# Optimization experiments

Measured on AMD Instinct MI355X. Metric: run time of the kernel, lower is better.

Reference implementation:

```python
import jax, jax.numpy as jnp
import numpy as np

N = 100000
E = 1600000
D_IN = 128
D_HID = 128
D_OUT = 128
HEADS = 4
NEG_SLOPE = 0.2  # PyG GATConv default leaky_relu slope


def setup_inputs() -> dict:
    key = jax.random.key(0)
    ks = jax.random.split(key, 16)
    ch1 = D_HID // HEADS
    ch2 = D_OUT // HEADS
    inp = {
        "x": jax.random.normal(ks[0], (N, D_IN), dtype=jnp.float32),
        "edge_index": jax.random.randint(ks[1], (2, E), 0, N, dtype=jnp.int64),
        # conv1 params
        "W1": jax.random.normal(ks[2], (D_IN, HEADS * ch1), dtype=jnp.float32) * 0.05,
        "a1_src": jax.random.normal(ks[3], (HEADS, ch1), dtype=jnp.float32) * 0.05,
        "a1_dst": jax.random.normal(ks[4], (HEADS, ch1), dtype=jnp.float32) * 0.05,
        "b1": jnp.zeros((HEADS * ch1,), dtype=jnp.float32),
        # conv2 params
        "W2": jax.random.normal(ks[5], (D_HID, HEADS * ch2), dtype=jnp.float32) * 0.05,
        "a2_src": jax.random.normal(ks[6], (HEADS, ch2), dtype=jnp.float32) * 0.05,
        "a2_dst": jax.random.normal(ks[7], (HEADS, ch2), dtype=jnp.float32) * 0.05,
        "b2": jnp.zeros((HEADS * ch2,), dtype=jnp.float32),
        # residual linear
        "Wr": jax.random.normal(ks[8], (D_IN, D_OUT), dtype=jnp.float32) * 0.05,
        "br": jnp.zeros((D_OUT,), dtype=jnp.float32),
    }
    return inp


def _gat_conv(x, W, a_src, a_dst, bias, src, dst, n_nodes):
    """Single PyG-style GATConv (concat heads, eval-mode / no dropout).
    src/dst already include self loops. x: [N, Din]. Returns [N, H*C]."""
    H, C = a_src.shape
    h = (x @ W).reshape(n_nodes, H, C)                      # [N,H,C]
    s_src = jnp.einsum("nhc,hc->nh", h, a_src)              # [N,H]
    s_dst = jnp.einsum("nhc,hc->nh", h, a_dst)              # [N,H]
    e = s_src[src] + s_dst[dst]                             # [E',H]
    e = jnp.where(e > 0, e, NEG_SLOPE * e)                  # leaky_relu
    # softmax over edges grouped by destination node
    e_max = jax.ops.segment_max(e, dst, num_segments=n_nodes)  # [N,H]
    e_exp = jnp.exp(e - e_max[dst])
    denom = jax.ops.segment_sum(e_exp, dst, num_segments=n_nodes)  # [N,H]
    alpha = e_exp / denom[dst]                              # [E',H]
    msg = alpha[:, :, None] * h[src]                        # [E',H,C]
    out = jax.ops.segment_sum(msg, dst, num_segments=n_nodes)  # [N,H,C]
    return out.reshape(n_nodes, H * C) + bias


def reference(x, edge_index, W1, a1_src, a1_dst, b1, W2, a2_src, a2_dst, b2, Wr, br):
    n_nodes = x.shape[0]
    loops = jnp.arange(n_nodes, dtype=edge_index.dtype)
    src = jnp.concatenate([edge_index[0], loops])           # add_self_loops=True
    dst = jnp.concatenate([edge_index[1], loops])
    h1 = _gat_conv(x, W1, a1_src, a1_dst, b1, src, dst, n_nodes)
    h1 = jax.nn.relu(h1)
    h2 = _gat_conv(h1, W2, a2_src, a2_dst, b2, src, dst, n_nodes)
    return h2 + x @ Wr + br
```

## Files before the change

kernel.cpp:

```cpp
#include <hip/hip_runtime.h>

#define NEG_SLOPE 0.2f

typedef short bf16x8 __attribute__((ext_vector_type(8)));
typedef float f32x4 __attribute__((ext_vector_type(4)));

__device__ __forceinline__ float leaky1(float e) { return e > 0.f ? e : NEG_SLOPE * e; }

__device__ __forceinline__ unsigned short f2bf(float f) {
    unsigned u = __float_as_uint(f);
    u += 0x7fffu + ((u >> 16) & 1u);
    return (unsigned short)(u >> 16);
}

__device__ __forceinline__ void split2(float x, short& h, short& lo) {
    unsigned short hb_ = f2bf(x);
    float hf = __uint_as_float(((unsigned)hb_) << 16);
    h = (short)hb_;
    lo = (short)f2bf(x - hf);
}

#define EPB 4096

__global__ __launch_bounds__(256) void bucket_hist(const int* __restrict__ dst,
                                                   int* __restrict__ gcnt,
                                                   int* __restrict__ relBase,
                                                   int E, int N, int NB) {
    __shared__ int hist[256];
    int t = threadIdx.x, blk = blockIdx.x;
    if (t < NB) hist[t] = 0;
    __syncthreads();
    int e0 = blk * EPB + t;
#pragma unroll 4
    for (int k = 0; k < EPB / 256; ++k) {
        int e = e0 + k * 256;
        if (e < E) {
            int d = dst[e];
            if ((unsigned)d < (unsigned)N) atomicAdd(&hist[d >> 9], 1);
        }
    }
    __syncthreads();
    if (t < NB) relBase[blk * NB + t] = atomicAdd(&gcnt[t], hist[t]);
}

__global__ __launch_bounds__(256) void scan_buckets(const int* __restrict__ gcnt,
                                                    int* __restrict__ gboff, int NB) {
    __shared__ int sm[256];
    int t = threadIdx.x;
    int v = (t < NB) ? gcnt[t] : 0;
    sm[t] = v;
    __syncthreads();
#pragma unroll
    for (int o = 1; o < 256; o <<= 1) {
        int u = (t >= o) ? sm[t - o] : 0;
        __syncthreads();
        sm[t] += u;
        __syncthreads();
    }
    if (t < NB) gboff[t] = sm[t] - v;
    if (t == NB - 1) gboff[NB] = sm[t];
}

__global__ __launch_bounds__(256) void bucket_scatter(const int* __restrict__ src,
                                                      const int* __restrict__ dst,
                                                      const int* __restrict__ gboff,
                                                      const int* __restrict__ relBase,
                                                      int2* __restrict__ eb,
                                                      int E, int N, int NB) {
    __shared__ int cur[256];
    int t = threadIdx.x, blk = blockIdx.x;
    if (t < NB) cur[t] = gboff[t] + relBase[blk * NB + t];
    __syncthreads();
    int e0 = blk * EPB + t;
#pragma unroll 4
    for (int k = 0; k < EPB / 256; ++k) {
        int e = e0 + k * 256;
        if (e < E) {
            int d = dst[e];
            if ((unsigned)d < (unsigned)N) {
                int pos = atomicAdd(&cur[d >> 9], 1);
                eb[pos] = make_int2(src[e], d);
            }
        }
    }
}

__global__ __launch_bounds__(512) void csr_build(const int2* __restrict__ eb,
                                                 const int* __restrict__ gboff,
                                                 int* __restrict__ offs,
                                                 int* __restrict__ csr,
                                                 int N, int NB) {
    __shared__ int lcnt[512];
    __shared__ int sm[512];
    __shared__ int cur[512];
    int t = threadIdx.x, b = blockIdx.x;
    lcnt[t] = 0;
    __syncthreads();
    int s0 = gboff[b], s1 = gboff[b + 1];
    for (int e = s0 + t; e < s1; e += 512) atomicAdd(&lcnt[eb[e].y & 511], 1);
    __syncthreads();
    int v = lcnt[t];
    sm[t] = v;
    __syncthreads();
#pragma unroll
    for (int o = 1; o < 512; o <<= 1) {
        int u = (t >= o) ? sm[t - o] : 0;
        __syncthreads();
        sm[t] += u;
        __syncthreads();
    }
    int base = gboff[b] + sm[t] - v;
    cur[t] = base;
    int n0 = (b << 9) + t;
    if (n0 < N) offs[n0] = base;
    if (b == NB - 1 && t == 0) offs[N] = gboff[NB];
    __syncthreads();
    for (int e = s0 + t; e < s1; e += 512) {
        int2 p = eb[e];
        int pos = atomicAdd(&cur[p.y & 511], 1);
        csr[pos] = p.x;
    }
}


__global__ __launch_bounds__(256, 3) void gemm_mfma(const float* __restrict__ X,
                                                    const float* __restrict__ W,
                                                    float* __restrict__ OUT,
                                                    unsigned short* __restrict__ HB,
                                                    const float* __restrict__ bias,
                                                    int accumulate,
                                                    const float* __restrict__ ASrc,
                                                    const float* __restrict__ ADst,
                                                    float* __restrict__ sS4,
                                                    float* __restrict__ sD4, int N) {
    __shared__ __align__(16) char pool[49152];
    short* At2h = (short*)pool;
    short* At2l = (short*)(pool + 8192);
    short* Bt2h = (short*)(pool + 16384);
    short* Bt2l = (short*)(pool + 32768);
    float* outS = (float*)pool;

    int t = threadIdx.x;
    int row0 = blockIdx.x << 6;
    int l = t & 63, w = t >> 6, g = l >> 4, r = l & 15;
    int r0 = w << 4;

    f32x4 acc[8];
#pragma unroll
    for (int nb = 0; nb < 8; ++nb) acc[nb] = (f32x4){0.f, 0.f, 0.f, 0.f};

    int arow = t >> 2, aj = t & 3;
    int growA = row0 + arow;
    if (growA > N - 1) growA = N - 1;
    int bc = t & 127, bh4 = (t >> 7) << 2;

#pragma unroll 1
    for (int ph = 0; ph < 2; ++ph) {
        __syncthreads();
        {
            const float* xp = X + (size_t)growA * 128 + (ph << 6) + (aj << 4);
            float4 x0 = *(const float4*)(xp + 0);
            float4 x1 = *(const float4*)(xp + 4);
            float4 x2 = *(const float4*)(xp + 8);
            float4 x3 = *(const float4*)(xp + 12);
            float v[16] = {x0.x, x0.y, x0.z, x0.w, x1.x, x1.y, x1.z, x1.w,
                           x2.x, x2.y, x2.z, x2.w, x3.x, x3.y, x3.z, x3.w};
#pragma unroll
            for (int u = 0; u < 2; ++u) {
                bf16x8 hv, lv;
#pragma unroll
                for (int i = 0; i < 8; ++i) {
                    short hh, ll;
                    split2(v[u * 8 + i], hh, ll);
                    hv[i] = hh; lv[i] = ll;
                }
                int kg = 2 * aj + u;
                *(bf16x8*)&At2h[(kg * 64 + arow) * 8] = hv;
                *(bf16x8*)&At2l[(kg * 64 + arow) * 8] = lv;
            }
        }
        {
#pragma unroll
            for (int j = 0; j < 4; ++j) {
                int kg = bh4 + j;
                bf16x8 hv, lv;
#pragma unroll
                for (int i = 0; i < 8; ++i) {
                    float f = W[(size_t)((ph << 6) + (kg << 3) + i) * 128 + bc];
                    short hh, ll;
                    split2(f, hh, ll);
                    hv[i] = hh; lv[i] = ll;
                }
                *(bf16x8*)&Bt2h[(kg * 128 + bc) * 8] = hv;
                *(bf16x8*)&Bt2l[(kg * 128 + bc) * 8] = lv;
            }
        }
        __syncthreads();
#pragma unroll
        for (int m = 0; m < 2; ++m) {
            int kb = m << 2;
            bf16x8 ah = *(const bf16x8*)&At2h[((kb + g) * 64 + r0 + r) * 8];
            bf16x8 al = *(const bf16x8*)&At2l[((kb + g) * 64 + r0 + r) * 8];
#pragma unroll
            for (int nb = 0; nb < 8; ++nb) {
                bf16x8 bhv = *(const bf16x8*)&Bt2h[((kb + g) * 128 + (nb << 4) + r) * 8];
                bf16x8 blv = *(const bf16x8*)&Bt2l[((kb + g) * 128 + (nb << 4) + r) * 8];
                acc[nb] = __builtin_amdgcn_mfma_f32_16x16x32_bf16(ah, bhv, acc[nb], 0, 0, 0);
                acc[nb] = __builtin_amdgcn_mfma_f32_16x16x32_bf16(ah, blv, acc[nb], 0, 0, 0);
                acc[nb] = __builtin_amdgcn_mfma_f32_16x16x32_bf16(al, bhv, acc[nb], 0, 0, 0);
            }
        }
    }
    __syncthreads();
#pragma unroll
    for (int nb = 0; nb < 8; ++nb)
#pragma unroll
        for (int reg = 0; reg < 4; ++reg)
            outS[(r0 + (g << 2) + reg) * 129 + (nb << 4) + r] = acc[nb][reg];
    __syncthreads();
    int erow = t & 63, q = t >> 6;
    int grow = row0 + erow;
    if (grow < N) {
        float o[32];
#pragma unroll
        for (int i = 0; i < 32; ++i) o[i] = outS[erow * 129 + (q << 5) + i];
        if (bias) {
#pragma unroll
            for (int i = 0; i < 32; ++i) o[i] += bias[(q << 5) + i];
        }
        if (accumulate) {
#pragma unroll
            for (int i = 0; i < 8; ++i) {
                float4 old = *(const float4*)(OUT + (size_t)grow * 128 + (q << 5) + 4 * i);
                o[4 * i] += old.x; o[4 * i + 1] += old.y;
                o[4 * i + 2] += old.z; o[4 * i + 3] += old.w;
            }
        }
        if (OUT) {
#pragma unroll
            for (int i = 0; i < 8; ++i) {
                float4 v4 = make_float4(o[4 * i], o[4 * i + 1], o[4 * i + 2], o[4 * i + 3]);
                *(float4*)(OUT + (size_t)grow * 128 + (q << 5) + 4 * i) = v4;
            }
        }
        if (HB) {
#pragma unroll
            for (int u = 0; u < 4; ++u) {
                uint4 hv;
                hv.x = (unsigned)f2bf(o[8 * u + 0]) | ((unsigned)f2bf(o[8 * u + 1]) << 16);
                hv.y = (unsigned)f2bf(o[8 * u + 2]) | ((unsigned)f2bf(o[8 * u + 3]) << 16);
                hv.z = (unsigned)f2bf(o[8 * u + 4]) | ((unsigned)f2bf(o[8 * u + 5]) << 16);
                hv.w = (unsigned)f2bf(o[8 * u + 6]) | ((unsigned)f2bf(o[8 * u + 7]) << 16);
                *(uint4*)(HB + (size_t)grow * 128 + (q << 5) + 8 * u) = hv;
            }
        }
        if (ASrc) {
            float ps = 0.f, pd = 0.f;
#pragma unroll
            for (int i = 0; i < 32; ++i) {
                ps = fmaf(o[i], ASrc[(q << 5) + i], ps);
                pd = fmaf(o[i], ADst[(q << 5) + i], pd);
            }
            sS4[(size_t)grow * 4 + q] = ps;
            sD4[(size_t)grow * 4 + q] = pd;
        }
    }
}


__global__ __launch_bounds__(256) void agg7_kernel(const unsigned short* __restrict__ hb,
                                                   const float* __restrict__ sS4,
                                                   const float* __restrict__ sD4,
                                                   const int* __restrict__ offs,
                                                   const int* __restrict__ csr,
                                                   const float* __restrict__ bias,
                                                   float* __restrict__ out,
                                                   int do_relu, int N) {
    int n = (blockIdx.x << 2) + (threadIdx.x >> 6);
    if (n >= N) return;
    int lane = threadIdx.x & 63;
    int q    = lane >> 4;
    int cl   = lane & 15;
    int hd   = cl >> 2;
    unsigned clo = (unsigned)cl << 4;

    float sdh = sD4[(n << 2) + hd];
    float selfw = __expf(leaky1(sS4[(n << 2) + hd] + sdh));

    float acc[8] = {0.f, 0.f, 0.f, 0.f, 0.f, 0.f, 0.f, 0.f};
    float wsum = 0.f;

    int off = offs[n], end = offs[n + 1];
#pragma unroll 1
    for (int base = off; base < end; base += 16) {
        int e0 = base + q;
        int sj[4];
        float wj[4];
#pragma unroll
        for (int i = 0; i < 4; ++i) sj[i] = csr[e0 + (i << 2)];
#pragma unroll
        for (int i = 0; i < 4; ++i) {
            float s = sS4[((unsigned)sj[i] << 2) + hd] + sdh;
            float w = __expf(leaky1(s));
            wj[i] = (e0 + (i << 2) < end) ? w : 0.f;
        }
#pragma unroll
        for (int i = 0; i < 4; ++i) {
            uint4 v = *(const uint4*)((const char*)hb + (((unsigned)sj[i] << 8) + clo));
            float w = wj[i];
            wsum += w;
            acc[0] = fmaf(w, __uint_as_float(v.x << 16), acc[0]);
            acc[1] = fmaf(w, __uint_as_float(v.x & 0xffff0000u), acc[1]);
            acc[2] = fmaf(w, __uint_as_float(v.y << 16), acc[2]);
            acc[3] = fmaf(w, __uint_as_float(v.y & 0xffff0000u), acc[3]);
            acc[4] = fmaf(w, __uint_as_float(v.z << 16), acc[4]);
            acc[5] = fmaf(w, __uint_as_float(v.z & 0xffff0000u), acc[5]);
            acc[6] = fmaf(w, __uint_as_float(v.w << 16), acc[6]);
            acc[7] = fmaf(w, __uint_as_float(v.w & 0xffff0000u), acc[7]);
        }
    }
#pragma unroll
    for (int k = 0; k < 8; ++k) {
        acc[k] += __shfl_xor(acc[k], 16);
        acc[k] += __shfl_xor(acc[k], 32);
    }
    wsum += __shfl_xor(wsum, 16);
    wsum += __shfl_xor(wsum, 32);

    float iv = 1.0f / (wsum + selfw);

    if (q == 0) {
        uint4 hv = *(const uint4*)((const char*)hb + (((unsigned)n << 8) + clo));
        float hs[8];
        hs[0] = __uint_as_float(hv.x << 16);
        hs[1] = __uint_as_float(hv.x & 0xffff0000u);
        hs[2] = __uint_as_float(hv.y << 16);
        hs[3] = __uint_as_float(hv.y & 0xffff0000u);
        hs[4] = __uint_as_float(hv.z << 16);
        hs[5] = __uint_as_float(hv.z & 0xffff0000u);
        hs[6] = __uint_as_float(hv.w << 16);
        hs[7] = __uint_as_float(hv.w & 0xffff0000u);
        float4 b0 = *(const float4*)&bias[8 * cl];
        float4 b1 = *(const float4*)&bias[8 * cl + 4];
        float4 o0, o1;
        o0.x = fmaf(fmaf(selfw, hs[0], acc[0]), iv, b0.x);
        o0.y = fmaf(fmaf(selfw, hs[1], acc[1]), iv, b0.y);
        o0.z = fmaf(fmaf(selfw, hs[2], acc[2]), iv, b0.z);
        o0.w = fmaf(fmaf(selfw, hs[3], acc[3]), iv, b0.w);
        o1.x = fmaf(fmaf(selfw, hs[4], acc[4]), iv, b1.x);
        o1.y = fmaf(fmaf(selfw, hs[5], acc[5]), iv, b1.y);
        o1.z = fmaf(fmaf(selfw, hs[6], acc[6]), iv, b1.z);
        o1.w = fmaf(fmaf(selfw, hs[7], acc[7]), iv, b1.w);
        if (do_relu) {
            o0.x = fmaxf(o0.x, 0.f); o0.y = fmaxf(o0.y, 0.f);
            o0.z = fmaxf(o0.z, 0.f); o0.w = fmaxf(o0.w, 0.f);
            o1.x = fmaxf(o1.x, 0.f); o1.y = fmaxf(o1.y, 0.f);
            o1.z = fmaxf(o1.z, 0.f); o1.w = fmaxf(o1.w, 0.f);
        }
        *(float4*)(out + (size_t)n * 128 + 8 * cl) = o0;
        *(float4*)(out + (size_t)n * 128 + 8 * cl + 4) = o1;
    }
}


extern "C" void kernel_launch(void* const* d_in, const int* in_sizes, int n_in,
                              void* d_out, int out_size, void* d_ws, size_t ws_size,
                              hipStream_t stream) {
    const float* x   = (const float*)d_in[0];
    const int*   ei  = (const int*)d_in[1];
    const float* W1  = (const float*)d_in[2];
    const float* a1s = (const float*)d_in[3];
    const float* a1d = (const float*)d_in[4];
    const float* b1  = (const float*)d_in[5];
    const float* W2  = (const float*)d_in[6];
    const float* a2s = (const float*)d_in[7];
    const float* a2d = (const float*)d_in[8];
    const float* b2  = (const float*)d_in[9];
    const float* Wr  = (const float*)d_in[10];
    const float* br  = (const float*)d_in[11];
    float* out = (float*)d_out;

    int N = in_sizes[0] / 128;
    int E = in_sizes[1] / 2;
    const int* src = ei;
    const int* dst = ei + E;
    int NB = (N + 511) >> 9;
    int ebl = (E + EPB - 1) / EPB;

    char* w = (char*)d_ws;
    size_t p = 0;
    auto take = [&](size_t bytes) -> char* {
        char* r = w + p;
        p = (p + bytes + 255) & ~(size_t)255;
        return r;
    };
    float* bufB = (float*)take((size_t)N * 128 * 4);
    unsigned short* hb = (unsigned short*)take((size_t)N * 128 * 2);
    float* sS4  = (float*)take((size_t)N * 4 * 4);
    float* sD4  = (float*)take((size_t)N * 4 * 4);
    int* gcnt   = (int*)take((size_t)256 * 4);
    int* offs   = (int*)take((size_t)(N + 1) * 4);
    int* gboff  = (int*)take((size_t)257 * 4);
    int* relBase = (int*)take((size_t)ebl * NB * 4);
    int2* eb    = (int2*)take((size_t)E * 8);
    int* csr    = (int*)take((size_t)(E + 16) * 4);

    hipMemsetAsync(gcnt, 0, 256 * 4, stream);
    hipMemsetAsync(csr + E, 0, 16 * 4, stream);

    bucket_hist<<<ebl, 256, 0, stream>>>(dst, gcnt, relBase, E, N, NB);
    scan_buckets<<<1, 256, 0, stream>>>(gcnt, gboff, NB);
    bucket_scatter<<<ebl, 256, 0, stream>>>(src, dst, gboff, relBase, eb, E, N, NB);
    csr_build<<<NB, 512, 0, stream>>>(eb, gboff, offs, csr, N, NB);

    int gbm = (N + 63) >> 6;
    int ab = (N + 3) / 4;

    gemm_mfma<<<gbm, 256, 0, stream>>>(x, W1, nullptr, hb, nullptr, 0, a1s, a1d, sS4, sD4, N);
    agg7_kernel<<<ab, 256, 0, stream>>>(hb, sS4, sD4, offs, csr, b1, bufB, 1, N);
    gemm_mfma<<<gbm, 256, 0, stream>>>(bufB, W2, nullptr, hb, nullptr, 0, a2s, a2d, sS4, sD4, N);
    agg7_kernel<<<ab, 256, 0, stream>>>(hb, sS4, sD4, offs, csr, b2, out, 0, N);
    gemm_mfma<<<gbm, 256, 0, stream>>>(x, Wr, out, nullptr, br, 1, nullptr, nullptr, nullptr, nullptr, N);
}
```

Baseline: 425.4 us.

## Fuse residual GEMM into first GEMM, pack edge buckets, drop scan kernel

The residual projection x@Wr is now computed inside the first GEMM, which shares the converted x tiles and keeps a second accumulator set. The result goes to a residual buffer that the second aggregation adds in its epilogue, removing a separate GEMM pass that re-read x and read-modify-wrote the output. The bucket scan is folded into bucket_scatter and csr_build, and edge buckets are packed into 32-bit words (17-bit src, 9-bit local dst), removing a kernel launch and a memset and halving bucket traffic. Costs are more registers and LDS in the GEMM, a K-loop cut into smaller 32-wide phases, an extra N×128 float buffer round trip, and src limited to ids below 131072.

```diff
diff --git a/kernel.cpp b/kernel.cpp
--- a/kernel.cpp
+++ b/kernel.cpp
@@ -43,10 +43,15 @@
     if (t < NB) relBase[blk * NB + t] = atomicAdd(&gcnt[t], hist[t]);
 }
 
-__global__ __launch_bounds__(256) void scan_buckets(const int* __restrict__ gcnt,
-                                                    int* __restrict__ gboff, int NB) {
+__global__ __launch_bounds__(256) void bucket_scatter(const int* __restrict__ src,
+                                                      const int* __restrict__ dst,
+                                                      const int* __restrict__ gcnt,
+                                                      const int* __restrict__ relBase,
+                                                      int* __restrict__ eb,
+                                                      int E, int N, int NB) {
     __shared__ int sm[256];
-    int t = threadIdx.x;
+    __shared__ int cur[256];
+    int t = threadIdx.x, blk = blockIdx.x;
     int v = (t < NB) ? gcnt[t] : 0;
     sm[t] = v;
     __syncthreads();
@@ -57,19 +62,7 @@
         sm[t] += u;
         __syncthreads();
     }
-    if (t < NB) gboff[t] = sm[t] - v;
-    if (t == NB - 1) gboff[NB] = sm[t];
-}
-
-__global__ __launch_bounds__(256) void bucket_scatter(const int* __restrict__ src,
-                                                      const int* __restrict__ dst,
-                                                      const int* __restrict__ gboff,
-                                                      const int* __restrict__ relBase,
-                                                      int2* __restrict__ eb,
-                                                      int E, int N, int NB) {
-    __shared__ int cur[256];
-    int t = threadIdx.x, blk = blockIdx.x;
-    if (t < NB) cur[t] = gboff[t] + relBase[blk * NB + t];
+    if (t < NB) cur[t] = (sm[t] - v) + relBase[blk * NB + t];
     __syncthreads();
     int e0 = blk * EPB + t;
 #pragma unroll 4
@@ -79,25 +72,37 @@
             int d = dst[e];
             if ((unsigned)d < (unsigned)N) {
                 int pos = atomicAdd(&cur[d >> 9], 1);
-                eb[pos] = make_int2(src[e], d);
-            }
-        }
-    }
-}
-
-__global__ __launch_bounds__(512) void csr_build(const int2* __restrict__ eb,
-                                                 const int* __restrict__ gboff,
+                eb[pos] = (src[e] & 0x1FFFF) | ((d & 511) << 17);
+            }
+        }
+    }
+}
+
+__global__ __launch_bounds__(512) void csr_build(const int* __restrict__ eb,
+                                                 const int* __restrict__ gcnt,
                                                  int* __restrict__ offs,
                                                  int* __restrict__ csr,
                                                  int N, int NB) {
+    __shared__ int gsm[512];
     __shared__ int lcnt[512];
     __shared__ int sm[512];
     __shared__ int cur[512];
     int t = threadIdx.x, b = blockIdx.x;
+    int gv = (t < NB) ? gcnt[t] : 0;
+    gsm[t] = gv;
     lcnt[t] = 0;
     __syncthreads();
-    int s0 = gboff[b], s1 = gboff[b + 1];
-    for (int e = s0 + t; e < s1; e += 512) atomicAdd(&lcnt[eb[e].y & 511], 1);
+#pragma unroll
+    for (int o = 1; o < 512; o <<= 1) {
+        int u = (t >= o) ? gsm[t - o] : 0;
+        __syncthreads();
+        gsm[t] += u;
+        __syncthreads();
+    }
+    int s0 = (b == 0) ? 0 : gsm[b - 1];
+    int s1 = gsm[b];
+    int total = gsm[NB - 1];
+    for (int e = s0 + t; e < s1; e += 512) atomicAdd(&lcnt[(eb[e] >> 17) & 511], 1);
     __syncthreads();
     int v = lcnt[t];
     sm[t] = v;
@@ -109,35 +114,40 @@
         sm[t] += u;
         __syncthreads();
     }
-    int base = gboff[b] + sm[t] - v;
+    int base = s0 + sm[t] - v;
     cur[t] = base;
     int n0 = (b << 9) + t;
     if (n0 < N) offs[n0] = base;
-    if (b == NB - 1 && t == 0) offs[N] = gboff[NB];
+    if (b == NB - 1) {
+        if (t == 0) offs[N] = total;
+        if (t < 16) csr[total + t] = 0;
+    }
     __syncthreads();
     for (int e = s0 + t; e < s1; e += 512) {
-        int2 p = eb[e];
-        int pos = atomicAdd(&cur[p.y & 511], 1);
-        csr[pos] = p.x;
+        int p = eb[e];
+        int pos = atomicAdd(&cur[(p >> 17) & 511], 1);
+        csr[pos] = p & 0x1FFFF;
     }
 }
 
 
 __global__ __launch_bounds__(256, 3) void gemm_mfma(const float* __restrict__ X,
                                                     const float* __restrict__ W,
-                                                    float* __restrict__ OUT,
+                                                    const float* __restrict__ Wr,
                                                     unsigned short* __restrict__ HB,
-                                                    const float* __restrict__ bias,
-                                                    int accumulate,
+                                                    const float* __restrict__ rbias,
                                                     const float* __restrict__ ASrc,
                                                     const float* __restrict__ ADst,
                                                     float* __restrict__ sS4,
-                                                    float* __restrict__ sD4, int N) {
-    __shared__ __align__(16) char pool[49152];
-    short* At2h = (short*)pool;
-    short* At2l = (short*)(pool + 8192);
-    short* Bt2h = (short*)(pool + 16384);
-    short* Bt2l = (short*)(pool + 32768);
+                                                    float* __restrict__ sD4,
+                                                    float* __restrict__ R, int N) {
+    __shared__ __align__(16) char pool[40960];
+    short* Ah = (short*)pool;
+    short* Al = (short*)(pool + 4096);
+    short* Bh = (short*)(pool + 8192);
+    short* Bl = (short*)(pool + 16384);
+    short* Ch = (short*)(pool + 24576);
+    short* Cl = (short*)(pool + 32768);
     float* outS = (float*)pool;
 
     int t = threadIdx.x;
@@ -145,69 +155,85 @@
     int l = t & 63, w = t >> 6, g = l >> 4, r = l & 15;
     int r0 = w << 4;
 
-    f32x4 acc[8];
-#pragma unroll
-    for (int nb = 0; nb < 8; ++nb) acc[nb] = (f32x4){0.f, 0.f, 0.f, 0.f};
-
-    int arow = t >> 2, aj = t & 3;
+    f32x4 acc[8], accR[8];
+#pragma unroll
+    for (int nb = 0; nb < 8; ++nb) {
+        acc[nb] = (f32x4){0.f, 0.f, 0.f, 0.f};
+        accR[nb] = (f32x4){0.f, 0.f, 0.f, 0.f};
+    }
+
+    int arow = t >> 2, akg = t & 3;
     int growA = row0 + arow;
     if (growA > N - 1) growA = N - 1;
-    int bc = t & 127, bh4 = (t >> 7) << 2;
+    int bc = t & 127, bk0 = (t >> 7) << 1;
 
 #pragma unroll 1
-    for (int ph = 0; ph < 2; ++ph) {
+    for (int ph = 0; ph < 4; ++ph) {
         __syncthreads();
         {
-            const float* xp = X + (size_t)growA * 128 + (ph << 6) + (aj << 4);
+            const float* xp = X + (size_t)growA * 128 + (ph << 5) + (akg << 3);
             float4 x0 = *(const float4*)(xp + 0);
             float4 x1 = *(const float4*)(xp + 4);
-            float4 x2 = *(const float4*)(xp + 8);
-            float4 x3 = *(const float4*)(xp + 12);
-            float v[16] = {x0.x, x0.y, x0.z, x0.w, x1.x, x1.y, x1.z, x1.w,
-                           x2.x, x2.y, x2.z, x2.w, x3.x, x3.y, x3.z, x3.w};
-#pragma unroll
-            for (int u = 0; u < 2; ++u) {
+            float vv[8] = {x0.x, x0.y, x0.z, x0.w, x1.x, x1.y, x1.z, x1.w};
+            bf16x8 hv, lv;
+#pragma unroll
+            for (int i = 0; i < 8; ++i) {
+                short hh, ll;
+                split2(vv[i], hh, ll);
+                hv[i] = hh; lv[i] = ll;
+            }
+            *(bf16x8*)&Ah[(akg * 64 + arow) * 8] = hv;
+            *(bf16x8*)&Al[(akg * 64 + arow) * 8] = lv;
+        }
+#pragma unroll
+        for (int j = 0; j < 2; ++j) {
+            int kg = bk0 + j;
+            bf16x8 hv, lv;
+#pragma unroll
+            for (int i = 0; i < 8; ++i) {
+                float f = W[(size_t)((ph << 5) + (kg << 3) + i) * 128 + bc];
+                short hh, ll;
+                split2(f, hh, ll);
+                hv[i] = hh; lv[i] = ll;
+            }
+            *(bf16x8*)&Bh[(kg * 128 + bc) * 8] = hv;
+            *(bf16x8*)&Bl[(kg * 128 + bc) * 8] = lv;
+        }
+        if (Wr) {
+#pragma unroll
+            for (int j = 0; j < 2; ++j) {
+                int kg = bk0 + j;
                 bf16x8 hv, lv;
 #pragma unroll
                 for (int i = 0; i < 8; ++i) {
-                    short hh, ll;
-                    split2(v[u * 8 + i], hh, ll);
-                    hv[i] = hh; lv[i] = ll;
-                }
-                int kg = 2 * aj + u;
-                *(bf16x8*)&At2h[(kg * 64 + arow) * 8] = hv;
-                *(bf16x8*)&At2l[(kg * 64 + arow) * 8] = lv;
-            }
-        }
-        {
-#pragma unroll
-            for (int j = 0; j < 4; ++j) {
-                int kg = bh4 + j;
-                bf16x8 hv, lv;
-#pragma unroll
-                for (int i = 0; i < 8; ++i) {
-                    float f = W[(size_t)((ph << 6) + (kg << 3) + i) * 128 + bc];
+                    float f = Wr[(size_t)((ph << 5) + (kg << 3) + i) * 128 + bc];
                     short hh, ll;
                     split2(f, hh, ll);
                     hv[i] = hh; lv[i] = ll;
                 }
-                *(bf16x8*)&Bt2h[(kg * 128 + bc) * 8] = hv;
-                *(bf16x8*)&Bt2l[(kg * 128 + bc) * 8] = lv;
-            }
-        }
-        __syncthreads();
-#pragma unroll
-        for (int m = 0; m < 2; ++m) {
-            int kb = m << 2;
-            bf16x8 ah = *(const bf16x8*)&At2h[((kb + g) * 64 + r0 + r) * 8];
-            bf16x8 al = *(const bf16x8*)&At2l[((kb + g) * 64 + r0 + r) * 8];
+                *(bf16x8*)&Ch[(kg * 128 + bc) * 8] = hv;
+                *(bf16x8*)&Cl[(kg * 128 + bc) * 8] = lv;
+            }
+        }
+        __syncthreads();
+        bf16x8 ah = *(const bf16x8*)&Ah[(g * 64 + r0 + r) * 8];
+        bf16x8 al = *(const bf16x8*)&Al[(g * 64 + r0 + r) * 8];
+#pragma unroll
+        for (int nb = 0; nb < 8; ++nb) {
+            bf16x8 bhv = *(const bf16x8*)&Bh[(g * 128 + (nb << 4) + r) * 8];
+            bf16x8 blv = *(const bf16x8*)&Bl[(g * 128 + (nb << 4) + r) * 8];
+            acc[nb] = __builtin_amdgcn_mfma_f32_16x16x32_bf16(ah, bhv, acc[nb], 0, 0, 0);
+            acc[nb] = __builtin_amdgcn_mfma_f32_16x16x32_bf16(ah, blv, acc[nb], 0, 0, 0);
+            acc[nb] = __builtin_amdgcn_mfma_f32_16x16x32_bf16(al, bhv, acc[nb], 0, 0, 0);
+        }
+        if (Wr) {
 #pragma unroll
             for (int nb = 0; nb < 8; ++nb) {
-                bf16x8 bhv = *(const bf16x8*)&Bt2h[((kb + g) * 128 + (nb << 4) + r) * 8];
-                bf16x8 blv = *(const bf16x8*)&Bt2l[((kb + g) * 128 + (nb << 4) + r) * 8];
-                acc[nb] = __builtin_amdgcn_mfma_f32_16x16x32_bf16(ah, bhv, acc[nb], 0, 0, 0);
-                acc[nb] = __builtin_amdgcn_mfma_f32_16x16x32_bf16(ah, blv, acc[nb], 0, 0, 0);
-                acc[nb] = __builtin_amdgcn_mfma_f32_16x16x32_bf16(al, bhv, acc[nb], 0, 0, 0);
+                bf16x8 chv = *(const bf16x8*)&Ch[(g * 128 + (nb << 4) + r) * 8];
+                bf16x8 clv = *(const bf16x8*)&Cl[(g * 128 + (nb << 4) + r) * 8];
+                accR[nb] = __builtin_amdgcn_mfma_f32_16x16x32_bf16(ah, chv, accR[nb], 0, 0, 0);
+                accR[nb] = __builtin_amdgcn_mfma_f32_16x16x32_bf16(ah, clv, accR[nb], 0, 0, 0);
+                accR[nb] = __builtin_amdgcn_mfma_f32_16x16x32_bf16(al, chv, accR[nb], 0, 0, 0);
             }
         }
     }
@@ -220,39 +246,18 @@
     __syncthreads();
     int erow = t & 63, q = t >> 6;
     int grow = row0 + erow;
+    float o[32];
+#pragma unroll
+    for (int i = 0; i < 32; ++i) o[i] = outS[erow * 129 + (q << 5) + i];
     if (grow < N) {
-        float o[32];
-#pragma unroll
-        for (int i = 0; i < 32; ++i) o[i] = outS[erow * 129 + (q << 5) + i];
-        if (bias) {
-#pragma unroll
-            for (int i = 0; i < 32; ++i) o[i] += bias[(q << 5) + i];
-        }
-        if (accumulate) {
-#pragma unroll
-            for (int i = 0; i < 8; ++i) {
-                float4 old = *(const float4*)(OUT + (size_t)grow * 128 + (q << 5) + 4 * i);
-                o[4 * i] += old.x; o[4 * i + 1] += old.y;
-                o[4 * i + 2] += old.z; o[4 * i + 3] += old.w;
-            }
-        }
-        if (OUT) {
-#pragma unroll
-            for (int i = 0; i < 8; ++i) {
-                float4 v4 = make_float4(o[4 * i], o[4 * i + 1], o[4 * i + 2], o[4 * i + 3]);
-                *(float4*)(OUT + (size_t)grow * 128 + (q << 5) + 4 * i) = v4;
-            }
-        }
-        if (HB) {
-#pragma unroll
-            for (int u = 0; u < 4; ++u) {
-                uint4 hv;
-                hv.x = (unsigned)f2bf(o[8 * u + 0]) | ((unsigned)f2bf(o[8 * u + 1]) << 16);
-                hv.y = (unsigned)f2bf(o[8 * u + 2]) | ((unsigned)f2bf(o[8 * u + 3]) << 16);
-                hv.z = (unsigned)f2bf(o[8 * u + 4]) | ((unsigned)f2bf(o[8 * u + 5]) << 16);
-                hv.w = (unsigned)f2bf(o[8 * u + 6]) | ((unsigned)f2bf(o[8 * u + 7]) << 16);
-                *(uint4*)(HB + (size_t)grow * 128 + (q << 5) + 8 * u) = hv;
-            }
+#pragma unroll
+        for (int u = 0; u < 4; ++u) {
+            uint4 hv;
+            hv.x = (unsigned)f2bf(o[8 * u + 0]) | ((unsigned)f2bf(o[8 * u + 1]) << 16);
+            hv.y = (unsigned)f2bf(o[8 * u + 2]) | ((unsigned)f2bf(o[8 * u + 3]) << 16);
+            hv.z = (unsigned)f2bf(o[8 * u + 4]) | ((unsigned)f2bf(o[8 * u + 5]) << 16);
+            hv.w = (unsigned)f2bf(o[8 * u + 6]) | ((unsigned)f2bf(o[8 * u + 7]) << 16);
+            *(uint4*)(HB + (size_t)grow * 128 + (q << 5) + 8 * u) = hv;
         }
         if (ASrc) {
             float ps = 0.f, pd = 0.f;
@@ -263,6 +268,26 @@
             }
             sS4[(size_t)grow * 4 + q] = ps;
             sD4[(size_t)grow * 4 + q] = pd;
+        }
+    }
+    if (Wr) {
+        __syncthreads();
+#pragma unroll
+        for (int nb = 0; nb < 8; ++nb)
+#pragma unroll
+            for (int reg = 0; reg < 4; ++reg)
+                outS[(r0 + (g << 2) + reg) * 129 + (nb << 4) + r] = accR[nb][reg];
+        __syncthreads();
+        if (grow < N) {
+#pragma unroll
+            for (int i = 0; i < 8; ++i) {
+                float4 v4;
+                v4.x = outS[erow * 129 + (q << 5) + 4 * i + 0] + rbias[(q << 5) + 4 * i + 0];
+                v4.y = outS[erow * 129 + (q << 5) + 4 * i + 1] + rbias[(q << 5) + 4 * i + 1];
+                v4.z = outS[erow * 129 + (q << 5) + 4 * i + 2] + rbias[(q << 5) + 4 * i + 2];
+                v4.w = outS[erow * 129 + (q << 5) + 4 * i + 3] + rbias[(q << 5) + 4 * i + 3];
+                *(float4*)(R + (size_t)grow * 128 + (q << 5) + 4 * i) = v4;
+            }
         }
     }
 }
@@ -274,6 +299,7 @@
                                                    const int* __restrict__ offs,
                                                    const int* __restrict__ csr,
                                                    const float* __restrict__ bias,
+                                                   const float* __restrict__ resid,
                                                    float* __restrict__ out,
                                                    int do_relu, int N) {
     int n = (blockIdx.x << 2) + (threadIdx.x >> 6);
@@ -351,6 +377,12 @@
         o1.y = fmaf(fmaf(selfw, hs[5], acc[5]), iv, b1.y);
         o1.z = fmaf(fmaf(selfw, hs[6], acc[6]), iv, b1.z);
         o1.w = fmaf(fmaf(selfw, hs[7], acc[7]), iv, b1.w);
+        if (resid) {
+            float4 r0v = *(const float4*)(resid + (size_t)n * 128 + 8 * cl);
+            float4 r1v = *(const float4*)(resid + (size_t)n * 128 + 8 * cl + 4);
+            o0.x += r0v.x; o0.y += r0v.y; o0.z += r0v.z; o0.w += r0v.w;
+            o1.x += r1v.x; o1.y += r1v.y; o1.z += r1v.z; o1.w += r1v.w;
+        }
         if (do_relu) {
             o0.x = fmaxf(o0.x, 0.f); o0.y = fmaxf(o0.y, 0.f);
             o0.z = fmaxf(o0.z, 0.f); o0.w = fmaxf(o0.w, 0.f);
@@ -395,30 +427,27 @@
         return r;
     };
     float* bufB = (float*)take((size_t)N * 128 * 4);
+    float* Rbuf = (float*)take((size_t)N * 128 * 4);
     unsigned short* hb = (unsigned short*)take((size_t)N * 128 * 2);
     float* sS4  = (float*)take((size_t)N * 4 * 4);
     float* sD4  = (float*)take((size_t)N * 4 * 4);
     int* gcnt   = (int*)take((size_t)256 * 4);
     int* offs   = (int*)take((size_t)(N + 1) * 4);
-    int* gboff  = (int*)take((size_t)257 * 4);
     int* relBase = (int*)take((size_t)ebl * NB * 4);
-    int2* eb    = (int2*)take((size_t)E * 8);
+    int* eb     = (int*)take((size_t)E * 4);
     int* csr    = (int*)take((size_t)(E + 16) * 4);
 
     hipMemsetAsync(gcnt, 0, 256 * 4, stream);
-    hipMemsetAsync(csr + E, 0, 16 * 4, stream);
 
     bucket_hist<<<ebl, 256, 0, stream>>>(dst, gcnt, relBase, E, N, NB);
-    scan_buckets<<<1, 256, 0, stream>>>(gcnt, gboff, NB);
-    bucket_scatter<<<ebl, 256, 0, stream>>>(src, dst, gboff, relBase, eb, E, N, NB);
-    csr_build<<<NB, 512, 0, stream>>>(eb, gboff, offs, csr, N, NB);
+    bucket_scatter<<<ebl, 256, 0, stream>>>(src, dst, gcnt, relBase, eb, E, N, NB);
+    csr_build<<<NB, 512, 0, stream>>>(eb, gcnt, offs, csr, N, NB);
 
     int gbm = (N + 63) >> 6;
     int ab = (N + 3) / 4;
 
-    gemm_mfma<<<gbm, 256, 0, stream>>>(x, W1, nullptr, hb, nullptr, 0, a1s, a1d, sS4, sD4, N);
-    agg7_kernel<<<ab, 256, 0, stream>>>(hb, sS4, sD4, offs, csr, b1, bufB, 1, N);
-    gemm_mfma<<<gbm, 256, 0, stream>>>(bufB, W2, nullptr, hb, nullptr, 0, a2s, a2d, sS4, sD4, N);
-    agg7_kernel<<<ab, 256, 0, stream>>>(hb, sS4, sD4, offs, csr, b2, out, 0, N);
-    gemm_mfma<<<gbm, 256, 0, stream>>>(x, Wr, out, nullptr, br, 1, nullptr, nullptr, nullptr, nullptr, N);
-}
+    gemm_mfma<<<gbm, 256, 0, stream>>>(x, W1, Wr, hb, br, a1s, a1d, sS4, sD4, Rbuf, N);
+    agg7_kernel<<<ab, 256, 0, stream>>>(hb, sS4, sD4, offs, csr, b1, nullptr, bufB, 1, N);
+    gemm_mfma<<<gbm, 256, 0, stream>>>(bufB, W2, nullptr, hb, nullptr, a2s, a2d, sS4, sD4, nullptr, N);
+    agg7_kernel<<<ab, 256, 0, stream>>>(hb, sS4, sD4, offs, csr, b2, Rbuf, out, 0, N);
+}
```

After: 474.0 us. 11.4% more time.
